# Kernel optimization log

Measured on AMD Instinct MI355X. Metric: run time of the kernel, lower is better.

The kernel has to match this reference:

```python
import jax, jax.numpy as jnp
import numpy as np

B, T, N, F, H, R = 4, 16, 512, 5, 64, 824
NEG = -1e9

def leaky(v):
    return jax.nn.leaky_relu(v, negative_slope=0.01)

def lstm_dir(x, Wih, Whh, bih, bhh):
    # x: [S, T, F]; PyTorch gate order i, f, g, o
    S = x.shape[0]
    Hh = Whh.shape[1]
    def step(carry, xt):
        h, c = carry
        gates = xt @ Wih.T + h @ Whh.T + (bih + bhh)  # [S, 4H]
        i, f, g, o = jnp.split(gates, 4, axis=-1)
        i = jax.nn.sigmoid(i); f = jax.nn.sigmoid(f)
        g = jnp.tanh(g); o = jax.nn.sigmoid(o)
        c = f * c + i * g
        h = o * jnp.tanh(c)
        return (h, c), h
    init = (jnp.zeros((S, Hh), x.dtype), jnp.zeros((S, Hh), x.dtype))
    _, hs = jax.lax.scan(step, init, jnp.swapaxes(x, 0, 1))  # [T, S, H]
    return hs

def setup_inputs() -> dict:
    key = jax.random.key(0)
    ks = jax.random.split(key, 25)
    s = 0.05
    d = {}
    d['x'] = jax.random.normal(ks[0], (B, T, N, F), jnp.float32)
    keep = jax.random.bernoulli(ks[1], 0.1, (N, N)) | jnp.eye(N, dtype=bool)
    d['rel_encoding'] = (jax.random.uniform(ks[2], (N, N, R), jnp.float32)
                         * keep[:, :, None].astype(jnp.float32))
    d['rel_mask'] = jnp.where(jnp.sum(d['rel_encoding'], axis=2) == 0.0,
                              jnp.float32(NEG), jnp.float32(0.0))
    for tag, i in (('f', 3), ('b', 7)):
        d['Wih_' + tag] = jax.random.normal(ks[i], (4 * H, F), jnp.float32) * s
        d['Whh_' + tag] = jax.random.normal(ks[i + 1], (4 * H, H), jnp.float32) * s
        d['bih_' + tag] = jax.random.normal(ks[i + 2], (4 * H,), jnp.float32) * s
        d['bhh_' + tag] = jax.random.normal(ks[i + 3], (4 * H,), jnp.float32) * s
    d['fc0_w'] = jax.random.normal(ks[11], (H, 2 * H), jnp.float32) * s
    d['fc0_b'] = jax.random.normal(ks[12], (H,), jnp.float32) * s
    d['fc1_w'] = jax.random.normal(ks[13], (1, R), jnp.float32) * s
    d['fc1_b'] = jax.random.normal(ks[14], (1,), jnp.float32) * s
    d['fc2_w'] = jax.random.normal(ks[15], (1, H), jnp.float32) * s
    d['fc2_b'] = jax.random.normal(ks[16], (1,), jnp.float32) * s
    d['fc3_w'] = jax.random.normal(ks[17], (1, H), jnp.float32) * s
    d['fc3_b'] = jax.random.normal(ks[18], (1,), jnp.float32) * s
    d['pred_w'] = jax.random.normal(ks[19], (1, 2 * H), jnp.float32) * s
    d['pred_b'] = jax.random.normal(ks[20], (1,), jnp.float32) * s
    d['all_one'] = jnp.ones((N, 1), jnp.float32)
    return d

def reference(x, rel_encoding, rel_mask,
              Wih_f, Whh_f, bih_f, bhh_f,
              Wih_b, Whh_b, bih_b, bhh_b,
              fc0_w, fc0_b, fc1_w, fc1_b, fc2_w, fc2_b, fc3_w, fc3_b,
              pred_w, pred_b, all_one):
    b, t, n, f = x.shape
    new_x = jnp.transpose(x, (0, 2, 1, 3)).reshape(b * n, t, f)  # [S, T, F]
    hs_f = lstm_dir(new_x, Wih_f, Whh_f, bih_f, bhh_f)            # [T, S, H]
    hs_b = lstm_dir(new_x[:, ::-1, :], Wih_b, Whh_b, bih_b, bhh_b)
    # out_rnn[:, -1, :] = [fwd h at t=T-1, bwd h at t=T-1 (= first bwd step)]
    last = jnp.concatenate([hs_f[-1], hs_b[0]], axis=-1)          # [S, 2H]
    out_rnn = leaky(last @ fc0_w.T + fc0_b)                       # dropout = identity (eval)
    output = out_rnn.reshape(b, n, -1)                            # [B, N, H]
    # relation weight: fc1 over [N, N, 824] -> [N, N]
    rel_weight = leaky(jnp.einsum('nmr,r->nm', rel_encoding, fc1_w[0]) + fc1_b[0])
    head = leaky(output @ fc2_w.T + fc2_b)                        # [B, N, 1]
    tail = leaky(output @ fc3_w.T + fc3_b)                        # [B, N, 1]
    weight = (jnp.einsum('bni,mi->bnm', head, all_one)
              + jnp.einsum('ni,bmi->bnm', all_one, tail)
              + rel_weight[None])                                 # [B, N, N]
    weight_masked = jax.nn.softmax(rel_mask[None] + weight, axis=-1)
    outputs_proped = jnp.einsum('bnm,bmh->bnh', weight_masked, output)
    concat = jnp.concatenate([output, outputs_proped], axis=-1)   # [B, N, 2H]
    prediction = leaky(concat @ pred_w.T + pred_b)                # [B, N, 1]
    return prediction.reshape(b, n, -1)
```

## Files before the change

kernel.cpp:

```cpp
#include <hip/hip_runtime.h>
#include <math.h>

#define TT 16
#define NN 512
#define FD 5
#define HH 64

__device__ __forceinline__ float sigmoidf_(float x) { return 1.0f / (1.0f + expf(-x)); }
__device__ __forceinline__ float leakyf_(float x)   { return x >= 0.0f ? x : 0.01f * x; }

__global__ __launch_bounds__(256) void k_lstm(
    const float* __restrict__ x,
    const float* __restrict__ Wih_f, const float* __restrict__ Whh_f,
    const float* __restrict__ bih_f, const float* __restrict__ bhh_f,
    const float* __restrict__ Wih_b,
    const float* __restrict__ bih_b, const float* __restrict__ bhh_b,
    const float* __restrict__ fc0_w, const float* __restrict__ fc0_b,
    const float* __restrict__ fc2_w, const float* __restrict__ fc2_b,
    const float* __restrict__ fc3_w, const float* __restrict__ fc3_b,
    float* __restrict__ ws_out, float* __restrict__ ws_head, float* __restrict__ ws_tail)
{
    __shared__ __align__(16) float h_lds[4 * 64];
    __shared__ __align__(16) float gate_lds[4 * 256];
    __shared__ __align__(16) float x_lds[4 * TT * FD];
    __shared__ __align__(16) float last_lds[4 * 128];

    const int tid  = threadIdx.x;
    const int j    = tid;
    const int seq0 = blockIdx.x * 4;

    for (int i = tid; i < 4 * TT * FD; i += 256) {
        int s = i / (TT * FD), r = i % (TT * FD);
        int t = r / FD, f = r % FD;
        int seq = seq0 + s;
        int b = seq >> 9, n = seq & 511;
        x_lds[i] = x[(((b * TT) + t) * NN + n) * FD + f];
    }
    h_lds[tid & 255] = 0.0f;
    float w[64];
    const float4* W4 = (const float4*)Whh_f;
#pragma unroll
    for (int q = 0; q < 16; ++q) {
        float4 v = W4[j * 16 + q];
        w[4 * q + 0] = v.x; w[4 * q + 1] = v.y; w[4 * q + 2] = v.z; w[4 * q + 3] = v.w;
    }
    float wih[FD];
#pragma unroll
    for (int f = 0; f < FD; ++f) wih[f] = Wih_f[j * FD + f];
    const float bsum = bih_f[j] + bhh_f[j];

    float c = 0.0f;
    __syncthreads();

    for (int t = 0; t < TT; ++t) {
#pragma unroll
        for (int s = 0; s < 4; ++s) {
            float acc = bsum;
#pragma unroll
            for (int q = 0; q < 16; ++q) {
                float4 hv = *(const float4*)&h_lds[s * 64 + q * 4];
                acc = fmaf(hv.x, w[4 * q + 0], acc);
                acc = fmaf(hv.y, w[4 * q + 1], acc);
                acc = fmaf(hv.z, w[4 * q + 2], acc);
                acc = fmaf(hv.w, w[4 * q + 3], acc);
            }
#pragma unroll
            for (int f = 0; f < FD; ++f)
                acc = fmaf(x_lds[s * (TT * FD) + t * FD + f], wih[f], acc);
            gate_lds[s * 256 + j] = acc;
        }
        __syncthreads();
        {
            int s = tid >> 6, k = tid & 63;
            float gi = gate_lds[s * 256 + k];
            float gf = gate_lds[s * 256 + 64 + k];
            float gg = gate_lds[s * 256 + 128 + k];
            float go = gate_lds[s * 256 + 192 + k];
            float ii = sigmoidf_(gi), ff = sigmoidf_(gf);
            float gv = tanhf(gg),     oo = sigmoidf_(go);
            c = ff * c + ii * gv;
            h_lds[s * 64 + k] = oo * tanhf(c);
        }
        __syncthreads();
    }

    {
        float wb[FD];
#pragma unroll
        for (int f = 0; f < FD; ++f) wb[f] = Wih_b[j * FD + f];
        float bb = bih_b[j] + bhh_b[j];
#pragma unroll
        for (int s = 0; s < 4; ++s) {
            float acc = bb;
#pragma unroll
            for (int f = 0; f < FD; ++f)
                acc = fmaf(x_lds[s * (TT * FD) + (TT - 1) * FD + f], wb[f], acc);
            gate_lds[s * 256 + j] = acc;
        }
    }
    __syncthreads();
    {
        int s = tid >> 6, k = tid & 63;
        float gi = gate_lds[s * 256 + k];
        float gg = gate_lds[s * 256 + 128 + k];
        float go = gate_lds[s * 256 + 192 + k];
        float cb = sigmoidf_(gi) * tanhf(gg);
        float hb = sigmoidf_(go) * tanhf(cb);
        last_lds[s * 128 + k]      = h_lds[s * 64 + k];
        last_lds[s * 128 + 64 + k] = hb;
    }
    __syncthreads();

    {
        int s = tid >> 6, k = tid & 63;
        float acc = fc0_b[k];
        const float4* fw4 = (const float4*)fc0_w;
        const float4* l4  = (const float4*)&last_lds[s * 128];
#pragma unroll 8
        for (int q = 0; q < 32; ++q) {
            float4 wv = fw4[k * 32 + q];
            float4 lv = l4[q];
            acc = fmaf(lv.x, wv.x, acc);
            acc = fmaf(lv.y, wv.y, acc);
            acc = fmaf(lv.z, wv.z, acc);
            acc = fmaf(lv.w, wv.w, acc);
        }
        float o = leakyf_(acc);
        int seq = seq0 + s;
        ws_out[seq * 64 + k] = o;

        float ph = o * fc2_w[k];
        float pt = o * fc3_w[k];
#pragma unroll
        for (int m = 32; m >= 1; m >>= 1) {
            ph += __shfl_xor(ph, m);
            pt += __shfl_xor(pt, m);
        }
        if (k == 0) {
            ws_head[seq] = leakyf_(ph + fc2_b[0]);
            ws_tail[seq] = leakyf_(pt + fc3_b[0]);
        }
    }
}

__global__ __launch_bounds__(256) void k_rel(
    const float* __restrict__ rel_enc, const float* __restrict__ rel_mask,
    const float* __restrict__ fc1_w, const float* __restrict__ fc1_b,
    float* __restrict__ ws_rel)
{
    const int lane = threadIdx.x & 63;
    const int wave = (int)((blockIdx.x * 256 + threadIdx.x) >> 6);
    const long base = (long)wave * 64;

    float mask = rel_mask[base + lane];
    unsigned long long bal = __ballot(mask > -0.5f);

    float4 fw[4];
#pragma unroll
    for (int q = 0; q < 3; ++q) fw[q] = ((const float4*)fc1_w)[q * 64 + lane];
    if (lane < 14) fw[3] = ((const float4*)fc1_w)[3 * 64 + lane];
    const float b0 = fc1_b[0];

    while (bal) {
        int bit = __builtin_ctzll(bal);
        bal &= bal - 1;
        long m = base + bit;
        const float4* r4 = (const float4*)(rel_enc + m * 824);
        float acc = 0.0f;
#pragma unroll
        for (int q = 0; q < 3; ++q) {
            float4 v = r4[q * 64 + lane];
            acc = fmaf(v.x, fw[q].x, acc);
            acc = fmaf(v.y, fw[q].y, acc);
            acc = fmaf(v.z, fw[q].z, acc);
            acc = fmaf(v.w, fw[q].w, acc);
        }
        if (lane < 14) {
            float4 v = r4[3 * 64 + lane];
            acc = fmaf(v.x, fw[3].x, acc);
            acc = fmaf(v.y, fw[3].y, acc);
            acc = fmaf(v.z, fw[3].z, acc);
            acc = fmaf(v.w, fw[3].w, acc);
        }
#pragma unroll
        for (int s = 32; s >= 1; s >>= 1) acc += __shfl_xor(acc, s);
        if (lane == 0) ws_rel[m] = leakyf_(acc + b0);
    }
}

__global__ __launch_bounds__(256) void k_prop(
    const float* __restrict__ rel_mask,
    const float* __restrict__ ws_rel,
    const float* __restrict__ ws_out,
    const float* __restrict__ ws_head, const float* __restrict__ ws_tail,
    const float* __restrict__ pred_w, const float* __restrict__ pred_b,
    float* __restrict__ out)
{
    __shared__ float p_lds[4 * 512];
    const int lane = threadIdx.x & 63;
    const int wid  = threadIdx.x >> 6;
    const int row  = blockIdx.x * 4 + wid;
    const int b = row >> 9, n = row & 511;

    const float hd = ws_head[row];
    float wv[8];
    unsigned okm = 0u;
    float wmax = -INFINITY;
#pragma unroll
    for (int u = 0; u < 8; ++u) {
        int m = lane + 64 * u;
        float msk = rel_mask[n * 512 + m];
        float wgt = 0.0f;
        if (msk > -0.5f) {
            wgt = hd + ws_tail[b * 512 + m] + ws_rel[n * 512 + m];
            wmax = fmaxf(wmax, wgt);
            okm |= 1u << u;
        }
        wv[u] = wgt;
    }
#pragma unroll
    for (int s = 32; s >= 1; s >>= 1) wmax = fmaxf(wmax, __shfl_xor(wmax, s));

    float A = 0.0f;
#pragma unroll
    for (int u = 0; u < 8; ++u) {
        int m = lane + 64 * u;
        float p = 0.0f;
        if (okm & (1u << u)) p = expf(wv[u] - wmax);
        p_lds[wid * 512 + m] = p;
        A += p;
    }
#pragma unroll
    for (int s = 32; s >= 1; s >>= 1) A += __shfl_xor(A, s);
    __syncthreads();

    float acc = 0.0f;
    for (int m = 0; m < 512; ++m) {
        float p = p_lds[wid * 512 + m];
        if (p != 0.0f)
            acc = fmaf(p, ws_out[(b * 512 + m) * 64 + lane], acc);
    }
    float prop = acc / A;
    float o = ws_out[row * 64 + lane];
    float part = o * pred_w[lane] + prop * pred_w[64 + lane];
#pragma unroll
    for (int s = 32; s >= 1; s >>= 1) part += __shfl_xor(part, s);
    if (lane == 0) out[row] = leakyf_(part + pred_b[0]);
}

extern "C" void kernel_launch(void* const* d_in, const int* in_sizes, int n_in,
                              void* d_out, int out_size, void* d_ws, size_t ws_size,
                              hipStream_t stream)
{
    const float* x        = (const float*)d_in[0];
    const float* rel_enc  = (const float*)d_in[1];
    const float* rel_mask = (const float*)d_in[2];
    const float* Wih_f = (const float*)d_in[3];
    const float* Whh_f = (const float*)d_in[4];
    const float* bih_f = (const float*)d_in[5];
    const float* bhh_f = (const float*)d_in[6];
    const float* Wih_b = (const float*)d_in[7];
    const float* bih_b = (const float*)d_in[9];
    const float* bhh_b = (const float*)d_in[10];
    const float* fc0_w = (const float*)d_in[11];
    const float* fc0_b = (const float*)d_in[12];
    const float* fc1_w = (const float*)d_in[13];
    const float* fc1_b = (const float*)d_in[14];
    const float* fc2_w = (const float*)d_in[15];
    const float* fc2_b = (const float*)d_in[16];
    const float* fc3_w = (const float*)d_in[17];
    const float* fc3_b = (const float*)d_in[18];
    const float* pred_w = (const float*)d_in[19];
    const float* pred_b = (const float*)d_in[20];

    float* ws      = (float*)d_ws;
    float* ws_out  = ws;
    float* ws_head = ws_out + 2048 * 64;
    float* ws_tail = ws_head + 2048;
    float* ws_rel  = ws_tail + 2048;

    k_rel <<<1024, 256, 0, stream>>>(rel_enc, rel_mask, fc1_w, fc1_b, ws_rel);
    k_lstm<<<512,  256, 0, stream>>>(x, Wih_f, Whh_f, bih_f, bhh_f, Wih_b, bih_b, bhh_b,
                                     fc0_w, fc0_b, fc2_w, fc2_b, fc3_w, fc3_b,
                                     ws_out, ws_head, ws_tail);
    k_prop<<<512,  256, 0, stream>>>(rel_mask, ws_rel, ws_out, ws_head, ws_tail,
                                     pred_w, pred_b, (float*)d_out);
}
```

Measured before the change: 1.054 ms.

## Fuse relation and LSTM kernels into one launch; densify propagation loop

Merges the sparse relation-weight kernel and the LSTM kernel into a single grid: the first 1024 blocks compute the relation weights and the remaining blocks run the LSTM. This lets the memory-bound relation pass overlap with the latency-bound recurrence and removes one launch. The propagation kernel drops its block barrier, which is safe because each wave only uses its own LDS slice. It also replaces the zero-skipping branch with an unrolled dense FMA loop over all 512 neighbours, gaining loop-level parallelism at the cost of loading every neighbour row instead of only the roughly 10% that are nonzero.

```diff
diff --git a/kernel.cpp b/kernel.cpp
--- a/kernel.cpp
+++ b/kernel.cpp
@@ -9,7 +9,10 @@
 __device__ __forceinline__ float sigmoidf_(float x) { return 1.0f / (1.0f + expf(-x)); }
 __device__ __forceinline__ float leakyf_(float x)   { return x >= 0.0f ? x : 0.01f * x; }
 
-__global__ __launch_bounds__(256) void k_lstm(
+__global__ __launch_bounds__(256) void k_front(
+    const float* __restrict__ rel_enc, const float* __restrict__ rel_mask,
+    const float* __restrict__ fc1_w, const float* __restrict__ fc1_b,
+    float* __restrict__ ws_rel,
     const float* __restrict__ x,
     const float* __restrict__ Wih_f, const float* __restrict__ Whh_f,
     const float* __restrict__ bih_f, const float* __restrict__ bhh_f,
@@ -25,9 +28,52 @@
     __shared__ __align__(16) float x_lds[4 * TT * FD];
     __shared__ __align__(16) float last_lds[4 * 128];
 
-    const int tid  = threadIdx.x;
+    const int tid = threadIdx.x;
+
+    if (blockIdx.x < 1024) {
+        const int lane = tid & 63;
+        const int wave = (int)((blockIdx.x * 256 + tid) >> 6);
+        const long base = (long)wave * 64;
+
+        float mask = rel_mask[base + lane];
+        unsigned long long bal = __ballot(mask > -0.5f);
+
+        float4 fw[4];
+#pragma unroll
+        for (int q = 0; q < 3; ++q) fw[q] = ((const float4*)fc1_w)[q * 64 + lane];
+        if (lane < 14) fw[3] = ((const float4*)fc1_w)[3 * 64 + lane];
+        const float b0 = fc1_b[0];
+
+        while (bal) {
+            int bit = __builtin_ctzll(bal);
+            bal &= bal - 1;
+            long m = base + bit;
+            const float4* r4 = (const float4*)(rel_enc + m * 824);
+            float acc = 0.0f;
+#pragma unroll
+            for (int q = 0; q < 3; ++q) {
+                float4 v = r4[q * 64 + lane];
+                acc = fmaf(v.x, fw[q].x, acc);
+                acc = fmaf(v.y, fw[q].y, acc);
+                acc = fmaf(v.z, fw[q].z, acc);
+                acc = fmaf(v.w, fw[q].w, acc);
+            }
+            if (lane < 14) {
+                float4 v = r4[3 * 64 + lane];
+                acc = fmaf(v.x, fw[3].x, acc);
+                acc = fmaf(v.y, fw[3].y, acc);
+                acc = fmaf(v.z, fw[3].z, acc);
+                acc = fmaf(v.w, fw[3].w, acc);
+            }
+#pragma unroll
+            for (int s = 32; s >= 1; s >>= 1) acc += __shfl_xor(acc, s);
+            if (lane == 0) ws_rel[m] = leakyf_(acc + b0);
+        }
+        return;
+    }
+
     const int j    = tid;
-    const int seq0 = blockIdx.x * 4;
+    const int seq0 = (blockIdx.x - 1024) * 4;
 
     for (int i = tid; i < 4 * TT * FD; i += 256) {
         int s = i / (TT * FD), r = i % (TT * FD);
@@ -143,51 +189,6 @@
     }
 }
 
-__global__ __launch_bounds__(256) void k_rel(
-    const float* __restrict__ rel_enc, const float* __restrict__ rel_mask,
-    const float* __restrict__ fc1_w, const float* __restrict__ fc1_b,
-    float* __restrict__ ws_rel)
-{
-    const int lane = threadIdx.x & 63;
-    const int wave = (int)((blockIdx.x * 256 + threadIdx.x) >> 6);
-    const long base = (long)wave * 64;
-
-    float mask = rel_mask[base + lane];
-    unsigned long long bal = __ballot(mask > -0.5f);
-
-    float4 fw[4];
-#pragma unroll
-    for (int q = 0; q < 3; ++q) fw[q] = ((const float4*)fc1_w)[q * 64 + lane];
-    if (lane < 14) fw[3] = ((const float4*)fc1_w)[3 * 64 + lane];
-    const float b0 = fc1_b[0];
-
-    while (bal) {
-        int bit = __builtin_ctzll(bal);
-        bal &= bal - 1;
-        long m = base + bit;
-        const float4* r4 = (const float4*)(rel_enc + m * 824);
-        float acc = 0.0f;
-#pragma unroll
-        for (int q = 0; q < 3; ++q) {
-            float4 v = r4[q * 64 + lane];
-            acc = fmaf(v.x, fw[q].x, acc);
-            acc = fmaf(v.y, fw[q].y, acc);
-            acc = fmaf(v.z, fw[q].z, acc);
-            acc = fmaf(v.w, fw[q].w, acc);
-        }
-        if (lane < 14) {
-            float4 v = r4[3 * 64 + lane];
-            acc = fmaf(v.x, fw[3].x, acc);
-            acc = fmaf(v.y, fw[3].y, acc);
-            acc = fmaf(v.z, fw[3].z, acc);
-            acc = fmaf(v.w, fw[3].w, acc);
-        }
-#pragma unroll
-        for (int s = 32; s >= 1; s >>= 1) acc += __shfl_xor(acc, s);
-        if (lane == 0) ws_rel[m] = leakyf_(acc + b0);
-    }
-}
-
 __global__ __launch_bounds__(256) void k_prop(
     const float* __restrict__ rel_mask,
     const float* __restrict__ ws_rel,
@@ -232,16 +233,16 @@
     }
 #pragma unroll
     for (int s = 32; s >= 1; s >>= 1) A += __shfl_xor(A, s);
-    __syncthreads();
 
     float acc = 0.0f;
-    for (int m = 0; m < 512; ++m) {
-        float p = p_lds[wid * 512 + m];
-        if (p != 0.0f)
-            acc = fmaf(p, ws_out[(b * 512 + m) * 64 + lane], acc);
-    }
+    const float* wsrow = ws_out + ((long)b * 512) * 64 + lane;
+    const float* prow  = &p_lds[wid * 512];
+#pragma unroll 8
+    for (int m = 0; m < 512; ++m)
+        acc = fmaf(prow[m], wsrow[(long)m * 64], acc);
+
     float prop = acc / A;
-    float o = ws_out[row * 64 + lane];
+    float o = ws_out[(long)row * 64 + lane];
     float part = o * pred_w[lane] + prop * pred_w[64 + lane];
 #pragma unroll
     for (int s = 32; s >= 1; s >>= 1) part += __shfl_xor(part, s);
@@ -279,10 +280,10 @@
     float* ws_tail = ws_head + 2048;
     float* ws_rel  = ws_tail + 2048;
 
-    k_rel <<<1024, 256, 0, stream>>>(rel_enc, rel_mask, fc1_w, fc1_b, ws_rel);
-    k_lstm<<<512,  256, 0, stream>>>(x, Wih_f, Whh_f, bih_f, bhh_f, Wih_b, bih_b, bhh_b,
-                                     fc0_w, fc0_b, fc2_w, fc2_b, fc3_w, fc3_b,
-                                     ws_out, ws_head, ws_tail);
-    k_prop<<<512,  256, 0, stream>>>(rel_mask, ws_rel, ws_out, ws_head, ws_tail,
+    k_front<<<1536, 256, 0, stream>>>(rel_enc, rel_mask, fc1_w, fc1_b, ws_rel,
+                                      x, Wih_f, Whh_f, bih_f, bhh_f, Wih_b, bih_b, bhh_b,
+                                      fc0_w, fc0_b, fc2_w, fc2_b, fc3_w, fc3_b,
+                                      ws_out, ws_head, ws_tail);
+    k_prop <<<512, 256, 0, stream>>>(rel_mask, ws_rel, ws_out, ws_head, ws_tail,
                                      pred_w, pred_b, (float*)d_out);
 }
```

Measured after the change: 1.033 ms. 1.02x faster.
